# Optimization experiments

Measured on AMD Instinct MI355X. Metric: run time of the kernel, lower is better.

Reference implementation:

```python
import jax, jax.numpy as jnp
import numpy as np

B, C, H, W = 8, 256, 56, 56
R = 2
E = C // R  # embed_dim = in_channels // r


def setup_inputs() -> dict:
    key = jax.random.key(0)
    ks = jax.random.split(key, 10)
    s = 0.02
    return {
        "x": jax.random.normal(ks[0], (B, C, H, W), jnp.float32),
        "Wq": jax.random.normal(ks[1], (E, C), jnp.float32) * s,
        "bq": jax.random.normal(ks[2], (E,), jnp.float32) * s,
        "Wk": jax.random.normal(ks[3], (E, C), jnp.float32) * s,
        "bk": jax.random.normal(ks[4], (E,), jnp.float32) * s,
        "Wv": jax.random.normal(ks[5], (E, C), jnp.float32) * s,
        "bv": jax.random.normal(ks[6], (E,), jnp.float32) * s,
        "Wcat": jax.random.normal(ks[7], (1, 2 * E), jnp.float32) * s,  # 1x1 conv, no bias
        "Wexp": jax.random.normal(ks[8], (C, E), jnp.float32) * s,
        "bexp": jax.random.normal(ks[9], (C,), jnp.float32) * s,
    }


def reference(x, Wq, bq, Wk, bk, Wv, bv, Wcat, Wexp, bexp):
    b, c, h, w = x.shape
    n = h * w
    xf = x.reshape(b, c, n)  # 1x1 convs are channel matmuls over flattened pixels
    q = jnp.einsum('ec,bcn->ben', Wq, xf) + bq[None, :, None]   # [b,E,n]
    k = jnp.einsum('ec,bcn->ben', Wk, xf) + bk[None, :, None]   # [b,E,n]
    v = jnp.einsum('ec,bcn->bne', Wv, xf) + bv[None, None, :]   # [b,n,E]
    # concat_project 1x1 conv on qk=[q;k] repeated along a new n2 axis.
    # NOTE: source repeats BOTH q and k as 'b c n1 -> b c n1 n2', so the score
    # is constant along n2: s[b,n1] = ReLU(wq.q[:,n1] + wk.k[:,n1]).
    wq_c, wk_c = Wcat[0, :E], Wcat[0, E:]
    s = jax.nn.relu(jnp.einsum('e,ben->bn', wq_c, q)
                    + jnp.einsum('e,ben->bn', wk_c, k))         # [b,n]
    attn = jnp.broadcast_to(s[:, :, None], (b, n, n)) / n       # [b,n,n]
    embed = jnp.einsum('bij,bje->bie', attn, v)                 # [b,n,E]
    out = jnp.einsum('ce,bne->bcn', Wexp, embed) + bexp[None, :, None]
    return out.reshape(b, c, h, w) + x
```

## Files before the change

### kernel.cpp

```cpp
#include <hip/hip_runtime.h>

#define CC 256
#define EE 128
#define BB 8
#define NN 3136
#define NN4 784
#define T4 8
#define NTILES 98

__device__ __forceinline__ float waveReduceSum(float v) {
    #pragma unroll
    for (int off = 32; off > 0; off >>= 1) v += __shfl_down(v, off, 64);
    return v;
}

__global__ void __launch_bounds__(256) k1(
        const float* __restrict__ x,
        const float* __restrict__ Wq, const float* __restrict__ bq,
        const float* __restrict__ Wk, const float* __restrict__ bk,
        const float* __restrict__ Wv, const float* __restrict__ bv,
        const float* __restrict__ Wcat, const float* __restrict__ Wexp,
        float* __restrict__ xbar, float* __restrict__ Mg, float* __restrict__ hg,
        float* __restrict__ Ag, float* __restrict__ cst) {
    const int blk = blockIdx.x;
    const int tid = threadIdx.x;
    if (blk < BB * CC) {
        const float4* xr = (const float4*)(x + (size_t)blk * NN);
        float acc = 0.f;
        for (int i = tid; i < NN4; i += 256) {
            float4 v = xr[i];
            acc += (v.x + v.y) + (v.z + v.w);
        }
        acc = waveReduceSum(acc);
        __shared__ float red[4];
        int wid = tid >> 6, lane = tid & 63;
        if (lane == 0) red[wid] = acc;
        __syncthreads();
        if (tid == 0) xbar[blk] = (red[0] + red[1] + red[2] + red[3]) * (1.0f / NN);
    } else if (blk < BB * CC + CC) {
        int r = blk - BB * CC;
        __shared__ float we_s[EE];
        if (tid < EE) we_s[tid] = Wexp[r * EE + tid];
        __syncthreads();
        float m = 0.f;
        #pragma unroll 8
        for (int e = 0; e < EE; e++) m += we_s[e] * Wv[e * CC + tid];
        Mg[r * CC + tid] = m;
        if (tid < 64) {
            float hp = we_s[tid] * bv[tid] + we_s[tid + 64] * bv[tid + 64];
            hp = waveReduceSum(hp);
            if (tid == 0) hg[r] = hp;
        }
    } else {
        float a = 0.f;
        #pragma unroll 8
        for (int e = 0; e < EE; e++)
            a += Wcat[e] * Wq[e * CC + tid] + Wcat[EE + e] * Wk[e * CC + tid];
        Ag[tid] = a;
        if (tid < 64) {
            float cp = Wcat[tid] * bq[tid] + Wcat[tid + 64] * bq[tid + 64]
                     + Wcat[EE + tid] * bk[tid] + Wcat[EE + tid + 64] * bk[tid + 64];
            cp = waveReduceSum(cp);
            if (tid == 0) cst[0] = cp;
        }
    }
}

__global__ void __launch_bounds__(256) k2(
        const float* __restrict__ xbar, const float* __restrict__ Mg,
        const float* __restrict__ hg, float* __restrict__ gexp) {
    int w = threadIdx.x >> 6, lane = threadIdx.x & 63;
    int d = blockIdx.x * 4 + w;
    int b = d >> 8, c = d & 255;
    const float* Mr = Mg + c * CC;
    const float* xb = xbar + b * CC;
    float acc = Mr[lane]       * xb[lane]
              + Mr[lane + 64]  * xb[lane + 64]
              + Mr[lane + 128] * xb[lane + 128]
              + Mr[lane + 192] * xb[lane + 192];
    acc = waveReduceSum(acc);
    if (lane == 0) gexp[d] = acc + hg[c];
}

__global__ void __launch_bounds__(256) k3(
        const float* __restrict__ x, const float* __restrict__ A,
        const float* __restrict__ cst, const float* __restrict__ gexp,
        const float* __restrict__ bexp, float* __restrict__ out) {
    int b = blockIdx.x / NTILES;
    int tile = blockIdx.x - b * NTILES;
    int tid = threadIdx.x;
    int i4l = tid & 7, cg = tid >> 3;

    __shared__ float A_s[CC];
    __shared__ float g_s[CC];
    __shared__ float be_s[CC];
    __shared__ float4 part[32][8];
    __shared__ float4 s_s[8];

    A_s[tid]  = A[tid];
    g_s[tid]  = gexp[b * CC + tid];
    be_s[tid] = bexp[tid];
    __syncthreads();

    const float4* x4 = (const float4*)x + (size_t)b * CC * NN4 + tile * T4;
    float4*       o4 = (float4*)out     + (size_t)b * CC * NN4 + tile * T4;

    float4 xc[8];
    float4 acc = make_float4(0.f, 0.f, 0.f, 0.f);
    #pragma unroll
    for (int j = 0; j < 8; j++) {
        int c = cg * 8 + j;
        float4 v = x4[(size_t)c * NN4 + i4l];
        xc[j] = v;
        float a = A_s[c];
        acc.x = fmaf(a, v.x, acc.x);
        acc.y = fmaf(a, v.y, acc.y);
        acc.z = fmaf(a, v.z, acc.z);
        acc.w = fmaf(a, v.w, acc.w);
    }
    part[cg][i4l] = acc;
    __syncthreads();
    if (tid < 8) {
        float4 sum = part[0][tid];
        #pragma unroll
        for (int g = 1; g < 32; g++) {
            float4 p = part[g][tid];
            sum.x += p.x; sum.y += p.y; sum.z += p.z; sum.w += p.w;
        }
        float cv = cst[0];
        float4 s;
        s.x = fmaxf(sum.x + cv, 0.f);
        s.y = fmaxf(sum.y + cv, 0.f);
        s.z = fmaxf(sum.z + cv, 0.f);
        s.w = fmaxf(sum.w + cv, 0.f);
        s_s[tid] = s;
    }
    __syncthreads();
    float4 sv = s_s[i4l];
    #pragma unroll
    for (int j = 0; j < 8; j++) {
        int c = cg * 8 + j;
        float g  = g_s[c];
        float be = be_s[c];
        float4 xv = xc[j];
        float4 o;
        o.x = fmaf(sv.x, g, xv.x) + be;
        o.y = fmaf(sv.y, g, xv.y) + be;
        o.z = fmaf(sv.z, g, xv.z) + be;
        o.w = fmaf(sv.w, g, xv.w) + be;
        o4[(size_t)c * NN4 + i4l] = o;
    }
}

extern "C" void kernel_launch(void* const* d_in, const int* in_sizes, int n_in,
                              void* d_out, int out_size, void* d_ws, size_t ws_size,
                              hipStream_t stream) {
    const float* x    = (const float*)d_in[0];
    const float* Wq   = (const float*)d_in[1];
    const float* bq   = (const float*)d_in[2];
    const float* Wk   = (const float*)d_in[3];
    const float* bk   = (const float*)d_in[4];
    const float* Wv   = (const float*)d_in[5];
    const float* bv   = (const float*)d_in[6];
    const float* Wcat = (const float*)d_in[7];
    const float* Wexp = (const float*)d_in[8];
    const float* bexp = (const float*)d_in[9];
    float* out = (float*)d_out;

    float* ws   = (float*)d_ws;
    float* xbar = ws;
    float* gexp = ws + 2048;
    float* A    = ws + 4096;
    float* cst  = ws + 4352;
    float* hg   = ws + 4368;
    float* Mg   = ws + 4624;

    k1<<<BB * CC + CC + 1, 256, 0, stream>>>(x, Wq, bq, Wk, bk, Wv, bv, Wcat, Wexp,
                                             xbar, Mg, hg, A, cst);
    k2<<<512, 256, 0, stream>>>(xbar, Mg, hg, gexp);
    k3<<<BB * NTILES, 256, 0, stream>>>(x, A, cst, gexp, bexp, out);
}
```

Measured before the change: 110.9 us.

## Fuse gexp matvec into output kernel and drop separate k2 launch

Removes the small k2 kernel by having every block of the output kernel recompute the per-channel gexp value itself, a 256x256 matvec against a transposed Mg matrix, so that reads are coalesced. The prep kernel now orders the light weight-folding blocks first, then the x row-mean blocks, and stores Mg transposed. The output kernel issues its x loads before the matvec so memory latency overlaps with it, and sets a launch-bounds occupancy hint. This saves one launch and its dependency gap, but each of the 784 blocks now reads the full 256 KB MgT matrix, adding redundant L2 traffic and compute.

```diff
diff --git a/kernel.cpp b/kernel.cpp
--- a/kernel.cpp
+++ b/kernel.cpp
@@ -14,44 +14,17 @@
     return v;
 }
 
-__global__ void __launch_bounds__(256) k1(
+__global__ void __launch_bounds__(256) kA(
         const float* __restrict__ x,
         const float* __restrict__ Wq, const float* __restrict__ bq,
         const float* __restrict__ Wk, const float* __restrict__ bk,
         const float* __restrict__ Wv, const float* __restrict__ bv,
         const float* __restrict__ Wcat, const float* __restrict__ Wexp,
-        float* __restrict__ xbar, float* __restrict__ Mg, float* __restrict__ hg,
+        float* __restrict__ xbar, float* __restrict__ MgT, float* __restrict__ hg,
         float* __restrict__ Ag, float* __restrict__ cst) {
     const int blk = blockIdx.x;
     const int tid = threadIdx.x;
-    if (blk < BB * CC) {
-        const float4* xr = (const float4*)(x + (size_t)blk * NN);
-        float acc = 0.f;
-        for (int i = tid; i < NN4; i += 256) {
-            float4 v = xr[i];
-            acc += (v.x + v.y) + (v.z + v.w);
-        }
-        acc = waveReduceSum(acc);
-        __shared__ float red[4];
-        int wid = tid >> 6, lane = tid & 63;
-        if (lane == 0) red[wid] = acc;
-        __syncthreads();
-        if (tid == 0) xbar[blk] = (red[0] + red[1] + red[2] + red[3]) * (1.0f / NN);
-    } else if (blk < BB * CC + CC) {
-        int r = blk - BB * CC;
-        __shared__ float we_s[EE];
-        if (tid < EE) we_s[tid] = Wexp[r * EE + tid];
-        __syncthreads();
-        float m = 0.f;
-        #pragma unroll 8
-        for (int e = 0; e < EE; e++) m += we_s[e] * Wv[e * CC + tid];
-        Mg[r * CC + tid] = m;
-        if (tid < 64) {
-            float hp = we_s[tid] * bv[tid] + we_s[tid + 64] * bv[tid + 64];
-            hp = waveReduceSum(hp);
-            if (tid == 0) hg[r] = hp;
-        }
-    } else {
+    if (blk == 0) {
         float a = 0.f;
         #pragma unroll 8
         for (int e = 0; e < EE; e++)
@@ -63,42 +36,56 @@
             cp = waveReduceSum(cp);
             if (tid == 0) cst[0] = cp;
         }
+    } else if (blk <= CC) {
+        const int r = blk - 1;
+        __shared__ float we_s[EE];
+        if (tid < EE) we_s[tid] = Wexp[r * EE + tid];
+        __syncthreads();
+        float m = 0.f;
+        #pragma unroll 8
+        for (int e = 0; e < EE; e++) m += we_s[e] * Wv[e * CC + tid];
+        MgT[tid * CC + r] = m;
+        if (tid < 64) {
+            float hp = we_s[tid] * bv[tid] + we_s[tid + 64] * bv[tid + 64];
+            hp = waveReduceSum(hp);
+            if (tid == 0) hg[r] = hp;
+        }
+    } else {
+        const int row = blk - (CC + 1);
+        const float4* xr = (const float4*)(x + (size_t)row * NN);
+        float acc = 0.f;
+        for (int i = tid; i < NN4; i += 256) {
+            float4 v = xr[i];
+            acc += (v.x + v.y) + (v.z + v.w);
+        }
+        acc = waveReduceSum(acc);
+        __shared__ float red[4];
+        int wid = tid >> 6, lane = tid & 63;
+        if (lane == 0) red[wid] = acc;
+        __syncthreads();
+        if (tid == 0) xbar[row] = (red[0] + red[1] + red[2] + red[3]) * (1.0f / NN);
     }
 }
 
-__global__ void __launch_bounds__(256) k2(
-        const float* __restrict__ xbar, const float* __restrict__ Mg,
-        const float* __restrict__ hg, float* __restrict__ gexp) {
-    int w = threadIdx.x >> 6, lane = threadIdx.x & 63;
-    int d = blockIdx.x * 4 + w;
-    int b = d >> 8, c = d & 255;
-    const float* Mr = Mg + c * CC;
-    const float* xb = xbar + b * CC;
-    float acc = Mr[lane]       * xb[lane]
-              + Mr[lane + 64]  * xb[lane + 64]
-              + Mr[lane + 128] * xb[lane + 128]
-              + Mr[lane + 192] * xb[lane + 192];
-    acc = waveReduceSum(acc);
-    if (lane == 0) gexp[d] = acc + hg[c];
-}
-
-__global__ void __launch_bounds__(256) k3(
-        const float* __restrict__ x, const float* __restrict__ A,
-        const float* __restrict__ cst, const float* __restrict__ gexp,
+__global__ void __launch_bounds__(256, 4) kB(
+        const float* __restrict__ x, const float* __restrict__ xbar,
+        const float* __restrict__ MgT, const float* __restrict__ hg,
+        const float* __restrict__ Ag, const float* __restrict__ cst,
         const float* __restrict__ bexp, float* __restrict__ out) {
-    int b = blockIdx.x / NTILES;
-    int tile = blockIdx.x - b * NTILES;
-    int tid = threadIdx.x;
-    int i4l = tid & 7, cg = tid >> 3;
+    const int b    = blockIdx.x / NTILES;
+    const int tile = blockIdx.x - b * NTILES;
+    const int tid  = threadIdx.x;
+    const int i4l = tid & 7, cgr = tid >> 3;
 
     __shared__ float A_s[CC];
+    __shared__ float xb_s[CC];
     __shared__ float g_s[CC];
     __shared__ float be_s[CC];
     __shared__ float4 part[32][8];
     __shared__ float4 s_s[8];
 
-    A_s[tid]  = A[tid];
-    g_s[tid]  = gexp[b * CC + tid];
+    A_s[tid]  = Ag[tid];
+    xb_s[tid] = xbar[b * CC + tid];
     be_s[tid] = bexp[tid];
     __syncthreads();
 
@@ -106,28 +93,37 @@
     float4*       o4 = (float4*)out     + (size_t)b * CC * NN4 + tile * T4;
 
     float4 xc[8];
-    float4 acc = make_float4(0.f, 0.f, 0.f, 0.f);
+    #pragma unroll
+    for (int j = 0; j < 8; j++)
+        xc[j] = x4[(size_t)(cgr * 8 + j) * NN4 + i4l];
+
+    float g = hg[tid];
+    #pragma unroll 8
+    for (int k = 0; k < CC; k++)
+        g = fmaf(MgT[k * CC + tid], xb_s[k], g);
+    g_s[tid] = g;
+
+    float4 acc4 = make_float4(0.f, 0.f, 0.f, 0.f);
     #pragma unroll
     for (int j = 0; j < 8; j++) {
-        int c = cg * 8 + j;
-        float4 v = x4[(size_t)c * NN4 + i4l];
-        xc[j] = v;
-        float a = A_s[c];
-        acc.x = fmaf(a, v.x, acc.x);
-        acc.y = fmaf(a, v.y, acc.y);
-        acc.z = fmaf(a, v.z, acc.z);
-        acc.w = fmaf(a, v.w, acc.w);
+        const float a = A_s[cgr * 8 + j];
+        const float4 v = xc[j];
+        acc4.x = fmaf(a, v.x, acc4.x);
+        acc4.y = fmaf(a, v.y, acc4.y);
+        acc4.z = fmaf(a, v.z, acc4.z);
+        acc4.w = fmaf(a, v.w, acc4.w);
     }
-    part[cg][i4l] = acc;
+    part[cgr][i4l] = acc4;
     __syncthreads();
+
     if (tid < 8) {
         float4 sum = part[0][tid];
         #pragma unroll
-        for (int g = 1; g < 32; g++) {
-            float4 p = part[g][tid];
+        for (int g2 = 1; g2 < 32; g2++) {
+            float4 p = part[g2][tid];
             sum.x += p.x; sum.y += p.y; sum.z += p.z; sum.w += p.w;
         }
-        float cv = cst[0];
+        const float cv = cst[0];
         float4 s;
         s.x = fmaxf(sum.x + cv, 0.f);
         s.y = fmaxf(sum.y + cv, 0.f);
@@ -136,18 +132,19 @@
         s_s[tid] = s;
     }
     __syncthreads();
-    float4 sv = s_s[i4l];
+
+    const float4 sv = s_s[i4l];
     #pragma unroll
     for (int j = 0; j < 8; j++) {
-        int c = cg * 8 + j;
-        float g  = g_s[c];
-        float be = be_s[c];
-        float4 xv = xc[j];
+        const int c = cgr * 8 + j;
+        const float gg = g_s[c];
+        const float be = be_s[c];
+        const float4 xv = xc[j];
         float4 o;
-        o.x = fmaf(sv.x, g, xv.x) + be;
-        o.y = fmaf(sv.y, g, xv.y) + be;
-        o.z = fmaf(sv.z, g, xv.z) + be;
-        o.w = fmaf(sv.w, g, xv.w) + be;
+        o.x = fmaf(sv.x, gg, xv.x) + be;
+        o.y = fmaf(sv.y, gg, xv.y) + be;
+        o.z = fmaf(sv.z, gg, xv.z) + be;
+        o.w = fmaf(sv.w, gg, xv.w) + be;
         o4[(size_t)c * NN4 + i4l] = o;
     }
 }
@@ -169,14 +166,12 @@
 
     float* ws   = (float*)d_ws;
     float* xbar = ws;
-    float* gexp = ws + 2048;
-    float* A    = ws + 4096;
-    float* cst  = ws + 4352;
-    float* hg   = ws + 4368;
-    float* Mg   = ws + 4624;
+    float* Ag   = ws + 2048;
+    float* cst  = ws + 2304;
+    float* hg   = ws + 2320;
+    float* MgT  = ws + 2576;
 
-    k1<<<BB * CC + CC + 1, 256, 0, stream>>>(x, Wq, bq, Wk, bk, Wv, bv, Wcat, Wexp,
-                                             xbar, Mg, hg, A, cst);
-    k2<<<512, 256, 0, stream>>>(xbar, Mg, hg, gexp);
-    k3<<<BB * NTILES, 256, 0, stream>>>(x, A, cst, gexp, bexp, out);
+    kA<<<1 + CC + BB * CC, 256, 0, stream>>>(x, Wq, bq, Wk, bk, Wv, bv, Wcat, Wexp,
+                                             xbar, MgT, hg, Ag, cst);
+    kB<<<BB * NTILES, 256, 0, stream>>>(x, xbar, MgT, hg, Ag, cst, bexp, out);
 }
```

Result: slower. 116.6 us (+5.1%).
